# Performance work log

Hardware: AMD Instinct MI355X
Metric: run time of the kernel (lower is better)

Reference implementation:

```python
import jax, jax.numpy as jnp
import numpy as np

C = 128
K = 5
M = 150000   # num vertices
NF = 300000  # num faces
D = 192      # volume side
NEG_SLOPE = 0.2


def _x_shift(K):
    # Exactly replicates the torch module's grid construction.
    grid = np.linspace(-K // 2, K // 2, K)
    grid_3d = np.stack(np.meshgrid(grid, grid, grid), axis=0).transpose(2, 1, 3, 0)
    return jnp.asarray(grid_3d.reshape(-1, 3), jnp.float32)  # [K^3, 3]


def _trilinear_border(vol, g):
    # vol: [D1, D2, D3]; g: [N, 3] normalized coords in (x, y, z) order
    # (x -> D3/W, y -> D2/H, z -> D1/D), align_corners=True, padding_mode='border'.
    D1, D2, D3 = vol.shape
    def pix(c, S):
        return jnp.clip((c + 1.0) * 0.5 * (S - 1), 0.0, S - 1.0)
    ix, iy, iz = pix(g[:, 0], D3), pix(g[:, 1], D2), pix(g[:, 2], D1)
    x0f, y0f, z0f = jnp.floor(ix), jnp.floor(iy), jnp.floor(iz)
    wx, wy, wz = ix - x0f, iy - y0f, iz - z0f
    x0 = x0f.astype(jnp.int32); y0 = y0f.astype(jnp.int32); z0 = z0f.astype(jnp.int32)
    x1 = jnp.minimum(x0 + 1, D3 - 1)
    y1 = jnp.minimum(y0 + 1, D2 - 1)
    z1 = jnp.minimum(z0 + 1, D1 - 1)
    c000 = vol[z0, y0, x0]; c001 = vol[z0, y0, x1]
    c010 = vol[z0, y1, x0]; c011 = vol[z0, y1, x1]
    c100 = vol[z1, y0, x0]; c101 = vol[z1, y0, x1]
    c110 = vol[z1, y1, x0]; c111 = vol[z1, y1, x1]
    c00 = c000 * (1 - wx) + c001 * wx
    c01 = c010 * (1 - wx) + c011 * wx
    c10 = c100 * (1 - wx) + c101 * wx
    c11 = c110 * (1 - wx) + c111 * wx
    c0 = c00 * (1 - wy) + c01 * wy
    c1 = c10 * (1 - wy) + c11 * wy
    return c0 * (1 - wz) + c1 * wz


def _leaky(x):
    return jnp.where(x >= 0, x, NEG_SLOPE * x)


def setup_inputs() -> dict:
    key = jax.random.key(0)
    ks = jax.random.split(key, 9)
    v = jax.random.uniform(ks[0], (1, M, 3), jnp.float32, -0.9, 0.9)
    f = jax.random.randint(ks[1], (1, NF, 3), 0, M, jnp.int32)
    V = jax.random.normal(ks[2], (1, 1, D, D, D), jnp.float32)
    def init(k, shape, fan):
        return jax.random.normal(k, shape, jnp.float32) / np.sqrt(fan).astype(np.float32)
    Wconv = init(ks[3], (C, 1, K, K, K), K ** 3)
    bconv = jnp.zeros((C,), jnp.float32)
    Wlfc = init(ks[4], (C, C), C)
    blfc = jnp.zeros((C,), jnp.float32)
    W1 = init(ks[5], (C, 6), 6)
    b1 = jnp.zeros((C,), jnp.float32)
    W2 = init(ks[6], (4 * C, 2 * C), 2 * C)
    b2 = jnp.zeros((4 * C,), jnp.float32)
    W3 = init(ks[7], (2 * C, 4 * C), 4 * C)
    b3 = jnp.zeros((2 * C,), jnp.float32)
    return dict(v=v, f=f, V=V, Wconv=Wconv, bconv=bconv, Wlfc=Wlfc, blfc=blfc,
                W1=W1, b1=b1, W2=W2, b2=b2, W3=W3, b3=b3)


def reference(v, f, V, Wconv, bconv, Wlfc, blfc, W1, b1, W2, b2, W3, b3):
    m = v.shape[1]
    D1, D2, D3 = V.shape[2], V.shape[3], V.shape[4]
    Dm = max(D1, D2, D3)
    rescale = jnp.array([D3 / Dm, D2 / Dm, D1 / Dm], jnp.float32)
    x_shift = _x_shift(K)  # [K^3, 3]

    # --- cube sampling (Q = n_scale = 1), done under no_grad in torch ---
    pts = (v[0][:, None, :] + x_shift / Dm * 2.0) / rescale  # [m, K^3, 3]
    cubes = _trilinear_border(V[0, 0], pts.reshape(-1, 3)).reshape(m, K ** 3)
    cubes = jax.lax.stop_gradient(cubes)

    # --- localconv: Conv3d with full-size kernel == GEMM over flattened cube ---
    z_local = cubes @ Wconv.reshape(C, -1).T + bconv      # [m, C]
    z_local = _leaky(z_local)
    z_local = _leaky(z_local @ Wlfc.T + blfc)             # [m, C]

    # --- vertex normals (area-weighted face-normal accumulation, pytorch3d style) ---
    faces = f[0]
    vv = v[0]
    p0, p1, p2 = vv[faces[:, 0]], vv[faces[:, 1]], vv[faces[:, 2]]
    fn = jnp.cross(p1 - p0, p2 - p0)
    vn = jnp.zeros_like(vv)
    vn = vn.at[faces[:, 0]].add(fn).at[faces[:, 1]].add(fn).at[faces[:, 2]].add(fn)
    vn = vn / jnp.maximum(jnp.linalg.norm(vn, axis=-1, keepdims=True), 1e-6)

    # --- point-wise MLP fusion ---
    x = jnp.concatenate([v, vn[None]], axis=2)            # [1, m, 6]
    z_point = _leaky(x @ W1.T + b1)                       # [1, m, C]
    z = jnp.concatenate([z_point, z_local[None]], axis=2) # [1, m, 2C]
    z = _leaky(z @ W2.T + b2)                             # [1, m, 4C]
    z = _leaky(z @ W3.T + b3)                             # [1, m, 2C]
    return z
```

## Files before the change

kernel.cpp:

```cpp
#include <hip/hip_runtime.h>
#include <hip/hip_fp16.h>

#define NEG_SLOPE 0.2f

using f16x8 = __attribute__((ext_vector_type(8))) _Float16;
using f32x4 = __attribute__((ext_vector_type(4))) float;

__device__ __forceinline__ float leakyf(float x) { return x >= 0.f ? x : NEG_SLOPE * x; }

__device__ __forceinline__ void gload_lds16(const void* g, void* l) {
    __builtin_amdgcn_global_load_lds(
        (const __attribute__((address_space(1))) unsigned int*)g,
        (__attribute__((address_space(3))) unsigned int*)l, 16, 0, 0);
}

#define MFMA16(a, b, c) __builtin_amdgcn_mfma_f32_16x16x32_f16(a, b, c, 0, 0, 0)

__global__ __launch_bounds__(256)
void fn_kernel(const float* __restrict__ v, const int* __restrict__ f,
               float4* __restrict__ fn4, int nf) {
    int i = blockIdx.x * 256 + threadIdx.x;
    if (i >= nf) return;
    int i0 = f[3 * i], i1 = f[3 * i + 1], i2 = f[3 * i + 2];
    float p0x = v[3 * i0], p0y = v[3 * i0 + 1], p0z = v[3 * i0 + 2];
    float ux = v[3 * i1] - p0x, uy = v[3 * i1 + 1] - p0y, uz = v[3 * i1 + 2] - p0z;
    float wx = v[3 * i2] - p0x, wy = v[3 * i2 + 1] - p0y, wz = v[3 * i2 + 2] - p0z;
    fn4[i] = make_float4(uy * wz - uz * wy, uz * wx - ux * wz, ux * wy - uy * wx, 0.f);
}

__global__ __launch_bounds__(256)
void inc_hist_kernel(const int* __restrict__ f, unsigned* __restrict__ gh, int NE) {
    __shared__ unsigned h[1024];
    const int t = threadIdx.x, blk = blockIdx.x;
    h[t] = 0; h[t + 256] = 0; h[t + 512] = 0; h[t + 768] = 0;
    __syncthreads();
    int base = blk * 4096;
#pragma unroll
    for (int k = 0; k < 16; ++k) {
        int idx = base + k * 256 + t;
        if (idx < NE) atomicAdd(&h[((unsigned)f[idx]) >> 8], 1u);
    }
    __syncthreads();
#pragma unroll
    for (int k = 0; k < 4; ++k) { int b = t + k * 256; gh[(size_t)blk * 1024 + b] = h[b]; }
}

__global__ __launch_bounds__(256)
void row_scan_kernel(unsigned* __restrict__ gh, unsigned* __restrict__ binTotals, int NB) {
    __shared__ unsigned s[256];
    __shared__ unsigned carrySh;
    const int bin = blockIdx.x, t = threadIdx.x;
    if (t == 0) carrySh = 0;
    __syncthreads();
    for (int base = 0; base < NB; base += 256) {
        unsigned c = carrySh;
        int i = base + t;
        unsigned val = (i < NB) ? gh[(size_t)i * 1024 + bin] : 0;
        s[t] = val;
        __syncthreads();
        for (int d = 1; d < 256; d <<= 1) {
            unsigned x = (t >= d) ? s[t - d] : 0;
            __syncthreads();
            s[t] += x;
            __syncthreads();
        }
        if (i < NB) gh[(size_t)i * 1024 + bin] = s[t] - val + c;
        if (t == 255) carrySh = c + s[255];
        __syncthreads();
    }
    if (t == 0) binTotals[bin] = carrySh;
}

__global__ __launch_bounds__(1024)
void bin_scan_kernel(const unsigned* __restrict__ binTotals, unsigned* __restrict__ binstart) {
    __shared__ unsigned s[1024];
    int t = threadIdx.x;
    unsigned val = binTotals[t];
    s[t] = val;
    __syncthreads();
    for (int d = 1; d < 1024; d <<= 1) {
        unsigned x = (t >= d) ? s[t - d] : 0;
        __syncthreads();
        s[t] += x;
        __syncthreads();
    }
    binstart[t] = s[t] - val;
    if (t == 1023) binstart[1024] = s[1023];
}

__global__ __launch_bounds__(256)
void inc_scatter_kernel(const int* __restrict__ f, const unsigned* __restrict__ gh,
                        const unsigned* __restrict__ binstart,
                        unsigned* __restrict__ sortedV, unsigned* __restrict__ sortedE,
                        int NE) {
    __shared__ unsigned loc[1024];
    const int t = threadIdx.x, blk = blockIdx.x;
#pragma unroll
    for (int k = 0; k < 4; ++k) {
        int b = t + k * 256;
        loc[b] = gh[(size_t)blk * 1024 + b] + binstart[b];
    }
    __syncthreads();
    int base = blk * 4096;
#pragma unroll
    for (int k = 0; k < 16; ++k) {
        int idx = base + k * 256 + t;
        if (idx < NE) {
            unsigned vv = (unsigned)f[idx];
            unsigned pos = atomicAdd(&loc[vv >> 8], 1u);
            sortedV[pos] = vv;
            sortedE[pos] = (unsigned)idx;
        }
    }
}

__global__ __launch_bounds__(256)
void vn_gather_kernel(const unsigned* __restrict__ sortedV, const unsigned* __restrict__ sortedE,
                      const float4* __restrict__ fn4, const unsigned* __restrict__ binstart,
                      float* __restrict__ vn, int M) {
    __shared__ float acc[768];
    const int t = threadIdx.x, b = blockIdx.x;
    acc[t] = 0.f; acc[t + 256] = 0.f; acc[t + 512] = 0.f;
    __syncthreads();
    unsigned s = binstart[b], e = binstart[b + 1];
    for (unsigned i = s + t; i < e; i += 256) {
        unsigned vv = sortedV[i];
        float4 fn = fn4[sortedE[i] / 3];
        int lv = (int)(vv & 255u) * 3;
        atomicAdd(&acc[lv + 0], fn.x);
        atomicAdd(&acc[lv + 1], fn.y);
        atomicAdd(&acc[lv + 2], fn.z);
    }
    __syncthreads();
    int gv = b * 256 + t;
    if (gv < M) {
        vn[3 * gv + 0] = acc[t * 3 + 0];
        vn[3 * gv + 1] = acc[t * 3 + 1];
        vn[3 * gv + 2] = acc[t * 3 + 2];
    }
}

__global__ __launch_bounds__(256)
void code_hist_kernel(const float* __restrict__ v, int* __restrict__ codes,
                      int* __restrict__ hist, int M) {
    int i = blockIdx.x * 256 + threadIdx.x;
    if (i >= M) return;
    int cx = min(max((int)((v[3 * i + 0] + 1.f) * 8.f), 0), 15);
    int cy = min(max((int)((v[3 * i + 1] + 1.f) * 8.f), 0), 15);
    int cz = min(max((int)((v[3 * i + 2] + 1.f) * 8.f), 0), 15);
    int code = 0;
#pragma unroll
    for (int b = 0; b < 4; ++b)
        code |= (((cx >> b) & 1) << (3 * b)) | (((cy >> b) & 1) << (3 * b + 1)) |
                (((cz >> b) & 1) << (3 * b + 2));
    codes[i] = code;
    atomicAdd(&hist[code], 1);
}

__global__ __launch_bounds__(1024)
void scan_kernel(const int* __restrict__ hist, int* __restrict__ offs) {
    __shared__ int s[1024];
    int t = threadIdx.x;
    int v0 = hist[4 * t], v1 = hist[4 * t + 1], v2 = hist[4 * t + 2], v3 = hist[4 * t + 3];
    int sum = v0 + v1 + v2 + v3;
    s[t] = sum;
    __syncthreads();
    for (int d = 1; d < 1024; d <<= 1) {
        int val = (t >= d) ? s[t - d] : 0;
        __syncthreads();
        s[t] += val;
        __syncthreads();
    }
    int excl = s[t] - sum;
    offs[4 * t + 0] = excl;
    offs[4 * t + 1] = excl + v0;
    offs[4 * t + 2] = excl + v0 + v1;
    offs[4 * t + 3] = excl + v0 + v1 + v2;
}

__global__ __launch_bounds__(256)
void scatter_kernel(const int* __restrict__ codes, int* __restrict__ offs,
                    int* __restrict__ perm, int M) {
    int i = blockIdx.x * 256 + threadIdx.x;
    if (i >= M) return;
    int pos = atomicAdd(&offs[codes[i]], 1);
    perm[pos] = i;
}

__global__ __launch_bounds__(256)
void sample_kernel(const float* __restrict__ v, const float* __restrict__ vol,
                   const int* __restrict__ perm,
                   __half* __restrict__ cubes, int m_start, int cnt, int nwg) {
    __shared__ float bbox[2][392];
    __shared__ int pi0[2][16];
    __shared__ float pw[2][16];
    const int half = threadIdx.x >> 7;
    const int q = threadIdx.x & 127;
    int q8 = nwg >> 3, r8 = nwg & 7;
    int xcd = blockIdx.x & 7, idxb = blockIdx.x >> 3;
    int bid = (xcd < r8 ? xcd * (q8 + 1) : r8 * (q8 + 1) + (xcd - r8) * q8) + idxb;
    int ml = bid * 2 + half;
    bool valid = ml < cnt;
    int m = valid ? perm[m_start + ml] : 0;

    if (valid && q < 15) {
        int axis = q / 5, idx = q - 5 * axis;
        float g = -3.f + 1.25f * (float)idx;
        float p = v[3 * m + axis] + g / 192.f * 2.f;
        float pos = fminf(fmaxf((p + 1.f) * 0.5f * 191.f, 0.f), 191.f);
        float fl = floorf(pos);
        pi0[half][q] = (int)fl;
        pw[half][q] = pos - fl;
    }
    __syncthreads();
    if (valid) {
        int xlo = pi0[half][0], ylo = pi0[half][5], zlo = pi0[half][10];
        for (int i = q; i < 392; i += 128) {
            int dx = i & 7;
            int dy = (i >> 3) % 7;
            int dz = i / 56;
            int X = min(xlo + dx, 191), Y = min(ylo + dy, 191), Z = min(zlo + dz, 191);
            bbox[half][i] = vol[Z * 36864 + Y * 192 + X];
        }
    }
    __syncthreads();
    if (!valid) return;
    __half* dst = cubes + (size_t)ml * 128;
    if (q >= 125) { dst[q] = __float2half(0.f); return; }
    int a = q % 5, b = (q / 5) % 5, c = q / 25;
    int xlo = pi0[half][0], ylo = pi0[half][5], zlo = pi0[half][10];
    int gx0 = pi0[half][a], gy0 = pi0[half][5 + b], gz0 = pi0[half][10 + c];
    float wxv = pw[half][a], wyv = pw[half][5 + b], wzv = pw[half][10 + c];
    int x0 = gx0 - xlo, y0 = gy0 - ylo, z0 = gz0 - zlo;
    int x1 = min(gx0 + 1, 191) - xlo;
    int y1 = min(gy0 + 1, 191) - ylo;
    int z1 = min(gz0 + 1, 191) - zlo;
    const float* bb = bbox[half];
    int b00 = (z0 * 7 + y0) * 8, b01 = (z0 * 7 + y1) * 8;
    int b10 = (z1 * 7 + y0) * 8, b11 = (z1 * 7 + y1) * 8;
    float c000 = bb[b00 + x0], c001 = bb[b00 + x1];
    float c010 = bb[b01 + x0], c011 = bb[b01 + x1];
    float c100 = bb[b10 + x0], c101 = bb[b10 + x1];
    float c110 = bb[b11 + x0], c111 = bb[b11 + x1];
    float omx = 1.f - wxv, omy = 1.f - wyv, omz = 1.f - wzv;
    float c00 = c000 * omx + c001 * wxv;
    float c01 = c010 * omx + c011 * wxv;
    float c10 = c100 * omx + c101 * wxv;
    float c11 = c110 * omx + c111 * wxv;
    float c0 = c00 * omy + c01 * wyv;
    float c1 = c10 * omy + c11 * wyv;
    dst[25 * a + 5 * b + c] = __float2half(c0 * omz + c1 * wzv);
}

__global__ __launch_bounds__(256)
void prep_weights(const float* __restrict__ Wconv, const float* __restrict__ Wlfc,
                  const float* __restrict__ W2, const float* __restrict__ W3,
                  __half* __restrict__ wpadh, __half* __restrict__ wlfch,
                  __half* __restrict__ w2h, __half* __restrict__ w3h) {
    int b = blockIdx.x, t = threadIdx.x;
    if (b < 64) {
        int i = b * 256 + t; int ch = i >> 7, k = i & 127;
        wpadh[i] = __float2half(k < 125 ? Wconv[ch * 125 + k] : 0.f);
    } else if (b < 128) {
        int i = (b - 64) * 256 + t; wlfch[i] = __float2half(Wlfc[i]);
    } else if (b < 640) {
        int i = (b - 128) * 256 + t; w2h[i] = __float2half(W2[i]);
    } else {
        int i = (b - 640) * 256 + t; w3h[i] = __float2half(W3[i]);
    }
}

__global__ __launch_bounds__(256)
void point_kernel(const float* __restrict__ v, const float* __restrict__ vn,
                  const int* __restrict__ perm,
                  const float* __restrict__ W1, const float* __restrict__ b1,
                  __half* __restrict__ zcat, int m_start, int cnt) {
    int ml = blockIdx.x * 2 + (threadIdx.x >> 7);
    if (ml >= cnt) return;
    int n = threadIdx.x & 127;
    int m = perm[m_start + ml];
    float x0 = v[3 * m], x1 = v[3 * m + 1], x2 = v[3 * m + 2];
    float nx = vn[3 * m], ny = vn[3 * m + 1], nz = vn[3 * m + 2];
    float nrm = fmaxf(sqrtf(nx * nx + ny * ny + nz * nz), 1e-6f);
    nx /= nrm; ny /= nrm; nz /= nrm;
    const float* w = W1 + n * 6;
    float z = b1[n] + x0 * w[0] + x1 * w[1] + x2 * w[2] + nx * w[3] + ny * w[4] + nz * w[5];
    zcat[(size_t)ml * 256 + n] = __float2half(leakyf(z));
}

__global__ __launch_bounds__(256)
void convlfc_kernel(const __half* __restrict__ cubes, const __half* __restrict__ wconvh,
                    const float* __restrict__ bconv, const __half* __restrict__ wlfch,
                    const float* __restrict__ blfc, __half* __restrict__ zcat) {
    __shared__ __half Zt[128 * 128];
    __shared__ __half As[128 * 64];
    __shared__ __half Bs[128 * 64];
    const int t = threadIdx.x;
    const int lane = t & 63, wave = t >> 6;
    const int lr = lane & 15, lg = lane >> 4;
    const int wm = wave >> 1, wn = wave & 1;
    const int m0 = blockIdx.x * 128;
    const int srow = t >> 3;
    const int scb = ((t & 7) << 4) ^ (((t >> 3) & 7) << 4);
    const int swz = (lr & 7) << 4;

    const __half* Ag = cubes + (size_t)(m0 + srow) * 128 + (scb >> 1);
    const __half* Bg = wconvh + (size_t)srow * 128 + (scb >> 1);
    __half* Al = As + wave * 512;
    __half* Bl = Bs + wave * 512;
    const char* aB = (const char*)As + (wm * 64 + lr) * 128;
    const char* bB = (const char*)Bs + (wn * 64 + lr) * 128;

    f32x4 acc[4][4] = {};
    for (int kc = 0; kc < 128; kc += 64) {
#pragma unroll
        for (int i = 0; i < 4; ++i) {
            gload_lds16(Ag + (size_t)i * 32 * 128 + kc, Al + i * 2048);
            gload_lds16(Bg + (size_t)i * 32 * 128 + kc, Bl + i * 2048);
        }
        __syncthreads();
#pragma unroll
        for (int kk = 0; kk < 2; ++kk) {
            const int ko = (kk * 64 + lg * 16) ^ swz;
            f16x8 af[4], bf[4];
#pragma unroll
            for (int fx = 0; fx < 4; ++fx) {
                af[fx] = *(const f16x8*)(aB + fx * 2048 + ko);
                bf[fx] = *(const f16x8*)(bB + fx * 2048 + ko);
            }
#pragma unroll
            for (int fm = 0; fm < 4; ++fm)
#pragma unroll
                for (int fn = 0; fn < 4; ++fn)
                    acc[fm][fn] = MFMA16(af[fm], bf[fn], acc[fm][fn]);
        }
        __syncthreads();
    }
#pragma unroll
    for (int fm = 0; fm < 4; ++fm) {
#pragma unroll
        for (int fn = 0; fn < 4; ++fn) {
            int col = wn * 64 + fn * 16 + lr;
            float bias = bconv[col];
#pragma unroll
            for (int r = 0; r < 4; ++r) {
                int row = wm * 64 + fm * 16 + lg * 4 + r;
                float val = leakyf(acc[fm][fn][r] + bias);
                *(__half*)((char*)Zt + row * 256 + ((2 * col) ^ ((row & 7) << 4))) = __float2half(val);
            }
        }
    }
    __syncthreads();

    const __half* Bg2 = wlfch + (size_t)srow * 128 + (scb >> 1);
    const char* zR = (const char*)Zt + (wm * 64 + lr) * 256;
    f32x4 acc2[4][4] = {};
    for (int kc = 0; kc < 128; kc += 64) {
#pragma unroll
        for (int i = 0; i < 4; ++i)
            gload_lds16(Bg2 + (size_t)i * 32 * 128 + kc, Bl + i * 2048);
        __syncthreads();
#pragma unroll
        for (int kk = 0; kk < 2; ++kk) {
            const int kb = kc * 2 + kk * 64 + lg * 16;
            const int ko = (kk * 64 + lg * 16) ^ swz;
            f16x8 af[4], bf[4];
#pragma unroll
            for (int fx = 0; fx < 4; ++fx) {
                af[fx] = *(const f16x8*)(zR + fx * 4096 + (kb ^ swz));
                bf[fx] = *(const f16x8*)(bB + fx * 2048 + ko);
            }
#pragma unroll
            for (int fm = 0; fm < 4; ++fm)
#pragma unroll
                for (int fn = 0; fn < 4; ++fn)
                    acc2[fm][fn] = MFMA16(af[fm], bf[fn], acc2[fm][fn]);
        }
        __syncthreads();
    }
#pragma unroll
    for (int fm = 0; fm < 4; ++fm) {
#pragma unroll
        for (int fn = 0; fn < 4; ++fn) {
            int col = wn * 64 + fn * 16 + lr;
            float bias = blfc[col];
#pragma unroll
            for (int r = 0; r < 4; ++r) {
                int row = m0 + wm * 64 + fm * 16 + lg * 4 + r;
                zcat[(size_t)row * 256 + 128 + col] = __float2half(leakyf(acc2[fm][fn][r] + bias));
            }
        }
    }
}

template<bool F32OUT>
__global__ __launch_bounds__(256)
void gemm_wide(const __half* __restrict__ A, const __half* __restrict__ W,
               const float* __restrict__ bias, void* __restrict__ outp,
               int K, int Meff, int OS, int OC, const int* __restrict__ rowmap) {
    __shared__ __half As[4096];
    __shared__ __half Bs[16384];
    const int t = threadIdx.x;
    const int lane = t & 63, wave = t >> 6;
    const int lr = lane & 15, lg = lane >> 4;
    const int m0 = blockIdx.x * 64, n0 = blockIdx.y * 256;

    const int srow = t >> 3;
    const int scb = ((t & 7) << 4) ^ (((t >> 3) & 7) << 4);
    const __half* Ag = A + (size_t)(m0 + srow) * K + (scb >> 1);
    const __half* Wg = W + (size_t)(n0 + srow) * K + (scb >> 1);
    __half* Al = As + wave * 512;
    __half* Bl = Bs + wave * 512;

    const int swz = (lr & 7) << 4;
    const char* aB = (const char*)As + lr * 128;
    const char* bB = (const char*)Bs + (wave * 64 + lr) * 128;
    const int k0 = (lg * 16) ^ swz;
    const int k1 = (64 + lg * 16) ^ swz;

    f32x4 acc[4][4] = {};

    for (int kc = 0; kc < K; kc += 64) {
#pragma unroll
        for (int i = 0; i < 2; ++i)
            gload_lds16(Ag + (size_t)i * 32 * K + kc, Al + i * 2048);
#pragma unroll
        for (int i = 0; i < 8; ++i)
            gload_lds16(Wg + (size_t)i * 32 * K + kc, Bl + i * 2048);
        __syncthreads();
        f16x8 af[4], bf[4];
#pragma unroll
        for (int fx = 0; fx < 4; ++fx) {
            af[fx] = *(const f16x8*)(aB + fx * 2048 + k0);
            bf[fx] = *(const f16x8*)(bB + fx * 2048 + k0);
        }
#pragma unroll
        for (int fm = 0; fm < 4; ++fm)
#pragma unroll
            for (int fn = 0; fn < 4; ++fn)
                acc[fm][fn] = MFMA16(af[fm], bf[fn], acc[fm][fn]);
#pragma unroll
        for (int fx = 0; fx < 4; ++fx) {
            af[fx] = *(const f16x8*)(aB + fx * 2048 + k1);
            bf[fx] = *(const f16x8*)(bB + fx * 2048 + k1);
        }
#pragma unroll
        for (int fm = 0; fm < 4; ++fm)
#pragma unroll
            for (int fn = 0; fn < 4; ++fn)
                acc[fm][fn] = MFMA16(af[fm], bf[fn], acc[fm][fn]);
        __syncthreads();
    }

    float bv[4];
#pragma unroll
    for (int fn = 0; fn < 4; ++fn) bv[fn] = bias[n0 + wave * 64 + fn * 16 + lr];
    const int rbase = m0 + lg * 4;
    const int cbase = OC + n0 + wave * 64 + lr;
#pragma unroll
    for (int fm = 0; fm < 4; ++fm) {
#pragma unroll
        for (int r = 0; r < 4; ++r) {
            int row = rbase + fm * 16 + r;
            if (row < Meff) {
                size_t orow = (size_t)(rowmap ? rowmap[row] : row);
#pragma unroll
                for (int fn = 0; fn < 4; ++fn) {
                    float val = leakyf(acc[fm][fn][r] + bv[fn]);
                    if (F32OUT)
                        ((float*)outp)[orow * OS + cbase + fn * 16] = val;
                    else
                        ((__half*)outp)[orow * OS + cbase + fn * 16] = __float2half(val);
                }
            }
        }
    }
}

extern "C" void kernel_launch(void* const* d_in, const int* in_sizes, int n_in,
                              void* d_out, int out_size, void* d_ws, size_t ws_size,
                              hipStream_t stream) {
    const float* v = (const float*)d_in[0];
    const int* f = (const int*)d_in[1];
    const float* vol = (const float*)d_in[2];
    const float* Wconv = (const float*)d_in[3];
    const float* bconv = (const float*)d_in[4];
    const float* Wlfc = (const float*)d_in[5];
    const float* blfc = (const float*)d_in[6];
    const float* W1 = (const float*)d_in[7];
    const float* b1 = (const float*)d_in[8];
    const float* W2 = (const float*)d_in[9];
    const float* b2 = (const float*)d_in[10];
    const float* W3 = (const float*)d_in[11];
    const float* b3 = (const float*)d_in[12];
    float* out = (float*)d_out;
    const int M = in_sizes[0] / 3;
    const int NF = in_sizes[1] / 3;
    const int NE = 3 * NF;
    const int NB = (NE + 4095) / 4096;

    char* base = (char*)d_ws;
    float* vn = (float*)base;
    size_t off = ((size_t)M * 12 + 255) & ~(size_t)255;
    int* codes = (int*)(base + off); off += ((size_t)M * 4 + 255) & ~(size_t)255;
    int* perm  = (int*)(base + off); off += ((size_t)M * 4 + 255) & ~(size_t)255;
    int* hist  = (int*)(base + off); off += 4096 * 4;
    int* offs  = (int*)(base + off); off += 4096 * 4;
    float4* fn4 = (float4*)(base + off); off += (size_t)NF * 16;
    unsigned* sortedV = (unsigned*)(base + off); off += ((size_t)NE * 4 + 255) & ~(size_t)255;
    unsigned* sortedE = (unsigned*)(base + off); off += ((size_t)NE * 4 + 255) & ~(size_t)255;
    unsigned* gh = (unsigned*)(base + off); off += ((size_t)1024 * NB * 4 + 255) & ~(size_t)255;
    unsigned* binstart = (unsigned*)(base + off); off += 1032 * 4;
    unsigned* binTotals = (unsigned*)(base + off); off += 1024 * 4;
    __half* wpadh = (__half*)(base + off); off += 32768;
    __half* wlfch = (__half*)(base + off); off += 32768;
    __half* w2h = (__half*)(base + off); off += 262144;
    __half* w3h = (__half*)(base + off); off += 262144;
    size_t avail = ws_size > off ? ws_size - off : 0;
    size_t Mpad = ((size_t)M + 127) & ~(size_t)127;
    size_t chm = (avail / 1792) & ~(size_t)127;
    if (chm > Mpad) chm = Mpad;
    if (chm < 128) chm = 128;
    __half* cubes = (__half*)(base + off);
    __half* zcat = cubes + chm * 128;
    __half* h = zcat + chm * 256;

    fn_kernel<<<(NF + 255) / 256, 256, 0, stream>>>(v, f, fn4, NF);
    inc_hist_kernel<<<NB, 256, 0, stream>>>(f, gh, NE);
    row_scan_kernel<<<1024, 256, 0, stream>>>(gh, binTotals, NB);
    bin_scan_kernel<<<1, 1024, 0, stream>>>(binTotals, binstart);
    inc_scatter_kernel<<<NB, 256, 0, stream>>>(f, gh, binstart, sortedV, sortedE, NE);
    vn_gather_kernel<<<(M + 255) / 256, 256, 0, stream>>>(sortedV, sortedE, fn4, binstart, vn, M);

    hipMemsetAsync(hist, 0, 4096 * 4, stream);
    code_hist_kernel<<<(M + 255) / 256, 256, 0, stream>>>(v, codes, hist, M);
    scan_kernel<<<1, 1024, 0, stream>>>(hist, offs);
    scatter_kernel<<<(M + 255) / 256, 256, 0, stream>>>(codes, offs, perm, M);
    prep_weights<<<1152, 256, 0, stream>>>(Wconv, Wlfc, W2, W3, wpadh, wlfch, w2h, w3h);

    for (size_t ms = 0; ms < (size_t)M; ms += chm) {
        size_t rem = (size_t)M - ms;
        int cnt = (int)(rem < chm ? rem : chm);
        int mb = (cnt + 127) / 128;
        int mb64 = (cnt + 63) / 64;
        int nblk = (cnt + 1) / 2;
        sample_kernel<<<nblk, 256, 0, stream>>>(v, vol, perm, cubes, (int)ms, cnt, nblk);
        convlfc_kernel<<<mb, 256, 0, stream>>>(cubes, wpadh, bconv, wlfch, blfc, zcat);
        point_kernel<<<(cnt + 1) / 2, 256, 0, stream>>>(v, vn, perm, W1, b1, zcat, (int)ms, cnt);
        gemm_wide<false><<<dim3(mb64, 2), 256, 0, stream>>>(zcat, w2h, b2, h, 256, mb64 * 64, 512, 0, nullptr);
        gemm_wide<true><<<dim3(mb64, 1), 256, 0, stream>>>(h, w3h, b3, out, 512, cnt, 256, 0, perm + ms);
    }
}
```

Baseline: 504.3 us.

## Double-buffer LDS tiles in gemm_wide and repack sample bbox gather

```diff
diff --git a/kernel.cpp b/kernel.cpp
--- a/kernel.cpp
+++ b/kernel.cpp
@@ -191,7 +191,7 @@
 void sample_kernel(const float* __restrict__ v, const float* __restrict__ vol,
                    const int* __restrict__ perm,
                    __half* __restrict__ cubes, int m_start, int cnt, int nwg) {
-    __shared__ float bbox[2][392];
+    __shared__ float bbox[2][448];
     __shared__ int pi0[2][16];
     __shared__ float pw[2][16];
     const int half = threadIdx.x >> 7;
@@ -215,12 +215,21 @@
     __syncthreads();
     if (valid) {
         int xlo = pi0[half][0], ylo = pi0[half][5], zlo = pi0[half][10];
-        for (int i = q; i < 392; i += 128) {
-            int dx = i & 7;
-            int dy = (i >> 3) % 7;
-            int dz = i / 56;
-            int X = min(xlo + dx, 191), Y = min(ylo + dy, 191), Z = min(zlo + dz, 191);
-            bbox[half][i] = vol[Z * 36864 + Y * 192 + X];
+        int j = q & 63;
+        int dy = j >> 3, dx = j & 7;
+        if (dy < 7) {
+            int X = min(xlo + dx, 191);
+            int Y = min(ylo + dy, 191);
+            int rowoff = dy * 9 + dx;
+            const float* volYX = vol + Y * 192 + X;
+#pragma unroll
+            for (int k = 0; k < 4; ++k) {
+                int pz = (q >> 6) + k * 2;
+                if (pz < 7) {
+                    int Z = min(zlo + pz, 191);
+                    bbox[half][pz * 63 + rowoff] = volYX[Z * 36864];
+                }
+            }
         }
     }
     __syncthreads();
@@ -236,8 +245,8 @@
     int y1 = min(gy0 + 1, 191) - ylo;
     int z1 = min(gz0 + 1, 191) - zlo;
     const float* bb = bbox[half];
-    int b00 = (z0 * 7 + y0) * 8, b01 = (z0 * 7 + y1) * 8;
-    int b10 = (z1 * 7 + y0) * 8, b11 = (z1 * 7 + y1) * 8;
+    int b00 = z0 * 63 + y0 * 9, b01 = z0 * 63 + y1 * 9;
+    int b10 = z1 * 63 + y0 * 9, b11 = z1 * 63 + y1 * 9;
     float c000 = bb[b00 + x0], c001 = bb[b00 + x1];
     float c010 = bb[b01 + x0], c011 = bb[b01 + x1];
     float c100 = bb[b10 + x0], c101 = bb[b10 + x1];
@@ -398,8 +407,8 @@
 void gemm_wide(const __half* __restrict__ A, const __half* __restrict__ W,
                const float* __restrict__ bias, void* __restrict__ outp,
                int K, int Meff, int OS, int OC, const int* __restrict__ rowmap) {
-    __shared__ __half As[4096];
-    __shared__ __half Bs[16384];
+    __shared__ __half As[2][4096];
+    __shared__ __half Bs[2][16384];
     const int t = threadIdx.x;
     const int lane = t & 63, wave = t >> 6;
     const int lr = lane & 15, lg = lane >> 4;
@@ -409,25 +418,41 @@
     const int scb = ((t & 7) << 4) ^ (((t >> 3) & 7) << 4);
     const __half* Ag = A + (size_t)(m0 + srow) * K + (scb >> 1);
     const __half* Wg = W + (size_t)(n0 + srow) * K + (scb >> 1);
-    __half* Al = As + wave * 512;
-    __half* Bl = Bs + wave * 512;
 
     const int swz = (lr & 7) << 4;
-    const char* aB = (const char*)As + lr * 128;
-    const char* bB = (const char*)Bs + (wave * 64 + lr) * 128;
+    const int aOff = lr * 128;
+    const int bOff = (wave * 64 + lr) * 128;
     const int k0 = (lg * 16) ^ swz;
     const int k1 = (64 + lg * 16) ^ swz;
 
     f32x4 acc[4][4] = {};
 
+    {
+        __half* Al = As[0] + wave * 512;
+        __half* Bl = Bs[0] + wave * 512;
+#pragma unroll
+        for (int i = 0; i < 2; ++i)
+            gload_lds16(Ag + (size_t)i * 32 * K, Al + i * 2048);
+#pragma unroll
+        for (int i = 0; i < 8; ++i)
+            gload_lds16(Wg + (size_t)i * 32 * K, Bl + i * 2048);
+    }
+    __syncthreads();
+
+    int cur = 0;
     for (int kc = 0; kc < K; kc += 64) {
-#pragma unroll
-        for (int i = 0; i < 2; ++i)
-            gload_lds16(Ag + (size_t)i * 32 * K + kc, Al + i * 2048);
-#pragma unroll
-        for (int i = 0; i < 8; ++i)
-            gload_lds16(Wg + (size_t)i * 32 * K + kc, Bl + i * 2048);
-        __syncthreads();
+        if (kc + 64 < K) {
+            __half* Al = As[cur ^ 1] + wave * 512;
+            __half* Bl = Bs[cur ^ 1] + wave * 512;
+#pragma unroll
+            for (int i = 0; i < 2; ++i)
+                gload_lds16(Ag + (size_t)i * 32 * K + kc + 64, Al + i * 2048);
+#pragma unroll
+            for (int i = 0; i < 8; ++i)
+                gload_lds16(Wg + (size_t)i * 32 * K + kc + 64, Bl + i * 2048);
+        }
+        const char* aB = (const char*)As[cur] + aOff;
+        const char* bB = (const char*)Bs[cur] + bOff;
         f16x8 af[4], bf[4];
 #pragma unroll
         for (int fx = 0; fx < 4; ++fx) {
@@ -450,6 +475,7 @@
             for (int fn = 0; fn < 4; ++fn)
                 acc[fm][fn] = MFMA16(af[fm], bf[fn], acc[fm][fn]);
         __syncthreads();
+        cur ^= 1;
     }
 
     float bv[4];
```

Measured after the change: 504.8 us. About the same (+0.1%).

## Merge independent prelude kernels into combined launches and restructure sample bbox loads

Applied to the files above, without the earlier changes.

```diff
diff --git a/kernel.cpp b/kernel.cpp
--- a/kernel.cpp
+++ b/kernel.cpp
@@ -17,75 +17,146 @@
 #define MFMA16(a, b, c) __builtin_amdgcn_mfma_f32_16x16x32_f16(a, b, c, 0, 0, 0)
 
 __global__ __launch_bounds__(256)
-void fn_kernel(const float* __restrict__ v, const int* __restrict__ f,
-               float4* __restrict__ fn4, int nf) {
-    int i = blockIdx.x * 256 + threadIdx.x;
-    if (i >= nf) return;
-    int i0 = f[3 * i], i1 = f[3 * i + 1], i2 = f[3 * i + 2];
-    float p0x = v[3 * i0], p0y = v[3 * i0 + 1], p0z = v[3 * i0 + 2];
-    float ux = v[3 * i1] - p0x, uy = v[3 * i1 + 1] - p0y, uz = v[3 * i1 + 2] - p0z;
-    float wx = v[3 * i2] - p0x, wy = v[3 * i2 + 1] - p0y, wz = v[3 * i2 + 2] - p0z;
-    fn4[i] = make_float4(uy * wz - uz * wy, uz * wx - ux * wz, ux * wy - uy * wx, 0.f);
-}
-
-__global__ __launch_bounds__(256)
-void inc_hist_kernel(const int* __restrict__ f, unsigned* __restrict__ gh, int NE) {
+void prelude1_kernel(const float* __restrict__ v, const int* __restrict__ f,
+                     float4* __restrict__ fn4, int NF, int NE,
+                     unsigned* __restrict__ gh, int fnB, int ihB, int chB,
+                     int* __restrict__ codes, int* __restrict__ hist, int M,
+                     const float* __restrict__ Wconv, const float* __restrict__ Wlfc,
+                     const float* __restrict__ W2, const float* __restrict__ W3,
+                     __half* __restrict__ wpadh, __half* __restrict__ wlfch,
+                     __half* __restrict__ w2h, __half* __restrict__ w3h) {
     __shared__ unsigned h[1024];
-    const int t = threadIdx.x, blk = blockIdx.x;
-    h[t] = 0; h[t + 256] = 0; h[t + 512] = 0; h[t + 768] = 0;
-    __syncthreads();
-    int base = blk * 4096;
-#pragma unroll
-    for (int k = 0; k < 16; ++k) {
-        int idx = base + k * 256 + t;
-        if (idx < NE) atomicAdd(&h[((unsigned)f[idx]) >> 8], 1u);
-    }
-    __syncthreads();
-#pragma unroll
-    for (int k = 0; k < 4; ++k) { int b = t + k * 256; gh[(size_t)blk * 1024 + b] = h[b]; }
-}
-
-__global__ __launch_bounds__(256)
-void row_scan_kernel(unsigned* __restrict__ gh, unsigned* __restrict__ binTotals, int NB) {
+    const int t = threadIdx.x;
+    int b = blockIdx.x;
+    if (b < fnB) {
+        int i = b * 256 + t;
+        if (i >= NF) return;
+        int i0 = f[3 * i], i1 = f[3 * i + 1], i2 = f[3 * i + 2];
+        float p0x = v[3 * i0], p0y = v[3 * i0 + 1], p0z = v[3 * i0 + 2];
+        float ux = v[3 * i1] - p0x, uy = v[3 * i1 + 1] - p0y, uz = v[3 * i1 + 2] - p0z;
+        float wx = v[3 * i2] - p0x, wy = v[3 * i2 + 1] - p0y, wz = v[3 * i2 + 2] - p0z;
+        fn4[i] = make_float4(uy * wz - uz * wy, uz * wx - ux * wz, ux * wy - uy * wx, 0.f);
+    } else if (b < fnB + ihB) {
+        int blk = b - fnB;
+        h[t] = 0; h[t + 256] = 0; h[t + 512] = 0; h[t + 768] = 0;
+        __syncthreads();
+        int base = blk * 4096;
+#pragma unroll
+        for (int k = 0; k < 16; ++k) {
+            int idx = base + k * 256 + t;
+            if (idx < NE) atomicAdd(&h[((unsigned)f[idx]) >> 8], 1u);
+        }
+        __syncthreads();
+#pragma unroll
+        for (int k = 0; k < 4; ++k) { int bb = t + k * 256; gh[(size_t)blk * 1024 + bb] = h[bb]; }
+    } else if (b < fnB + ihB + chB) {
+        int i = (b - fnB - ihB) * 256 + t;
+        if (i >= M) return;
+        int cx = min(max((int)((v[3 * i + 0] + 1.f) * 8.f), 0), 15);
+        int cy = min(max((int)((v[3 * i + 1] + 1.f) * 8.f), 0), 15);
+        int cz = min(max((int)((v[3 * i + 2] + 1.f) * 8.f), 0), 15);
+        int code = 0;
+#pragma unroll
+        for (int bb = 0; bb < 4; ++bb)
+            code |= (((cx >> bb) & 1) << (3 * bb)) | (((cy >> bb) & 1) << (3 * bb + 1)) |
+                    (((cz >> bb) & 1) << (3 * bb + 2));
+        codes[i] = code;
+        atomicAdd(&hist[code], 1);
+    } else {
+        int bw = b - fnB - ihB - chB;
+        if (bw < 64) {
+            int i = bw * 256 + t; int ch = i >> 7, k = i & 127;
+            wpadh[i] = __float2half(k < 125 ? Wconv[ch * 125 + k] : 0.f);
+        } else if (bw < 128) {
+            int i = (bw - 64) * 256 + t; wlfch[i] = __float2half(Wlfc[i]);
+        } else if (bw < 640) {
+            int i = (bw - 128) * 256 + t; w2h[i] = __float2half(W2[i]);
+        } else {
+            int i = (bw - 640) * 256 + t; w3h[i] = __float2half(W3[i]);
+        }
+    }
+}
+
+__global__ __launch_bounds__(256)
+void prelude2_kernel(unsigned* __restrict__ gh, unsigned* __restrict__ binTotals, int NB,
+                     const int* __restrict__ hist, int* __restrict__ offs) {
     __shared__ unsigned s[256];
     __shared__ unsigned carrySh;
-    const int bin = blockIdx.x, t = threadIdx.x;
-    if (t == 0) carrySh = 0;
-    __syncthreads();
-    for (int base = 0; base < NB; base += 256) {
-        unsigned c = carrySh;
-        int i = base + t;
-        unsigned val = (i < NB) ? gh[(size_t)i * 1024 + bin] : 0;
-        s[t] = val;
-        __syncthreads();
-        for (int d = 1; d < 256; d <<= 1) {
-            unsigned x = (t >= d) ? s[t - d] : 0;
+    const int t = threadIdx.x;
+    if (blockIdx.x < 1024) {
+        const int bin = blockIdx.x;
+        if (t == 0) carrySh = 0;
+        __syncthreads();
+        for (int base = 0; base < NB; base += 256) {
+            unsigned c = carrySh;
+            int i = base + t;
+            unsigned val = (i < NB) ? gh[(size_t)i * 1024 + bin] : 0;
+            s[t] = val;
             __syncthreads();
-            s[t] += x;
+            for (int d = 1; d < 256; d <<= 1) {
+                unsigned x = (t >= d) ? s[t - d] : 0;
+                __syncthreads();
+                s[t] += x;
+                __syncthreads();
+            }
+            if (i < NB) gh[(size_t)i * 1024 + bin] = s[t] - val + c;
+            if (t == 255) carrySh = c + s[255];
             __syncthreads();
         }
-        if (i < NB) gh[(size_t)i * 1024 + bin] = s[t] - val + c;
-        if (t == 255) carrySh = c + s[255];
-        __syncthreads();
-    }
-    if (t == 0) binTotals[bin] = carrySh;
-}
-
-__global__ __launch_bounds__(1024)
-void bin_scan_kernel(const unsigned* __restrict__ binTotals, unsigned* __restrict__ binstart) {
-    __shared__ unsigned s[1024];
-    int t = threadIdx.x;
-    unsigned val = binTotals[t];
-    s[t] = val;
-    __syncthreads();
-    for (int d = 1; d < 1024; d <<= 1) {
-        unsigned x = (t >= d) ? s[t - d] : 0;
-        __syncthreads();
-        s[t] += x;
-        __syncthreads();
-    }
-    binstart[t] = s[t] - val;
-    if (t == 1023) binstart[1024] = s[1023];
+        if (t == 0) binTotals[bin] = carrySh;
+    } else {
+        if (t == 0) carrySh = 0;
+        __syncthreads();
+        for (int base = 0; base < 4096; base += 256) {
+            unsigned c = carrySh;
+            unsigned val = (unsigned)hist[base + t];
+            s[t] = val;
+            __syncthreads();
+            for (int d = 1; d < 256; d <<= 1) {
+                unsigned x = (t >= d) ? s[t - d] : 0;
+                __syncthreads();
+                s[t] += x;
+                __syncthreads();
+            }
+            offs[base + t] = (int)(s[t] - val + c);
+            if (t == 255) carrySh = c + s[255];
+            __syncthreads();
+        }
+    }
+}
+
+__global__ __launch_bounds__(256)
+void prelude3_kernel(const unsigned* __restrict__ binTotals, unsigned* __restrict__ binstart,
+                     const int* __restrict__ codes, int* __restrict__ offs,
+                     int* __restrict__ perm, int M) {
+    __shared__ unsigned s[256];
+    __shared__ unsigned carrySh;
+    const int t = threadIdx.x;
+    if (blockIdx.x == 0) {
+        if (t == 0) carrySh = 0;
+        __syncthreads();
+        for (int base = 0; base < 1024; base += 256) {
+            unsigned c = carrySh;
+            unsigned val = binTotals[base + t];
+            s[t] = val;
+            __syncthreads();
+            for (int d = 1; d < 256; d <<= 1) {
+                unsigned x = (t >= d) ? s[t - d] : 0;
+                __syncthreads();
+                s[t] += x;
+                __syncthreads();
+            }
+            binstart[base + t] = s[t] - val + c;
+            if (t == 255) carrySh = c + s[255];
+            __syncthreads();
+        }
+        if (t == 0) binstart[1024] = carrySh;
+    } else {
+        int i = (blockIdx.x - 1) * 256 + t;
+        if (i >= M) return;
+        int pos = atomicAdd(&offs[codes[i]], 1);
+        perm[pos] = i;
+    }
 }
 
 __global__ __launch_bounds__(256)
@@ -141,57 +212,10 @@
 }
 
 __global__ __launch_bounds__(256)
-void code_hist_kernel(const float* __restrict__ v, int* __restrict__ codes,
-                      int* __restrict__ hist, int M) {
-    int i = blockIdx.x * 256 + threadIdx.x;
-    if (i >= M) return;
-    int cx = min(max((int)((v[3 * i + 0] + 1.f) * 8.f), 0), 15);
-    int cy = min(max((int)((v[3 * i + 1] + 1.f) * 8.f), 0), 15);
-    int cz = min(max((int)((v[3 * i + 2] + 1.f) * 8.f), 0), 15);
-    int code = 0;
-#pragma unroll
-    for (int b = 0; b < 4; ++b)
-        code |= (((cx >> b) & 1) << (3 * b)) | (((cy >> b) & 1) << (3 * b + 1)) |
-                (((cz >> b) & 1) << (3 * b + 2));
-    codes[i] = code;
-    atomicAdd(&hist[code], 1);
-}
-
-__global__ __launch_bounds__(1024)
-void scan_kernel(const int* __restrict__ hist, int* __restrict__ offs) {
-    __shared__ int s[1024];
-    int t = threadIdx.x;
-    int v0 = hist[4 * t], v1 = hist[4 * t + 1], v2 = hist[4 * t + 2], v3 = hist[4 * t + 3];
-    int sum = v0 + v1 + v2 + v3;
-    s[t] = sum;
-    __syncthreads();
-    for (int d = 1; d < 1024; d <<= 1) {
-        int val = (t >= d) ? s[t - d] : 0;
-        __syncthreads();
-        s[t] += val;
-        __syncthreads();
-    }
-    int excl = s[t] - sum;
-    offs[4 * t + 0] = excl;
-    offs[4 * t + 1] = excl + v0;
-    offs[4 * t + 2] = excl + v0 + v1;
-    offs[4 * t + 3] = excl + v0 + v1 + v2;
-}
-
-__global__ __launch_bounds__(256)
-void scatter_kernel(const int* __restrict__ codes, int* __restrict__ offs,
-                    int* __restrict__ perm, int M) {
-    int i = blockIdx.x * 256 + threadIdx.x;
-    if (i >= M) return;
-    int pos = atomicAdd(&offs[codes[i]], 1);
-    perm[pos] = i;
-}
-
-__global__ __launch_bounds__(256)
 void sample_kernel(const float* __restrict__ v, const float* __restrict__ vol,
                    const int* __restrict__ perm,
                    __half* __restrict__ cubes, int m_start, int cnt, int nwg) {
-    __shared__ float bbox[2][392];
+    __shared__ float bbox[2][448];
     __shared__ int pi0[2][16];
     __shared__ float pw[2][16];
     const int half = threadIdx.x >> 7;
@@ -215,12 +239,21 @@
     __syncthreads();
     if (valid) {
         int xlo = pi0[half][0], ylo = pi0[half][5], zlo = pi0[half][10];
-        for (int i = q; i < 392; i += 128) {
-            int dx = i & 7;
-            int dy = (i >> 3) % 7;
-            int dz = i / 56;
-            int X = min(xlo + dx, 191), Y = min(ylo + dy, 191), Z = min(zlo + dz, 191);
-            bbox[half][i] = vol[Z * 36864 + Y * 192 + X];
+        int j = q & 63;
+        int dy = j >> 3, dx = j & 7;
+        if (dy < 7) {
+            int X = min(xlo + dx, 191);
+            int Y = min(ylo + dy, 191);
+            int rowoff = dy * 9 + dx;
+            const float* volYX = vol + Y * 192 + X;
+#pragma unroll
+            for (int k = 0; k < 4; ++k) {
+                int pz = (q >> 6) + k * 2;
+                if (pz < 7) {
+                    int Z = min(zlo + pz, 191);
+                    bbox[half][pz * 63 + rowoff] = volYX[Z * 36864];
+                }
+            }
         }
     }
     __syncthreads();
@@ -236,8 +269,8 @@
     int y1 = min(gy0 + 1, 191) - ylo;
     int z1 = min(gz0 + 1, 191) - zlo;
     const float* bb = bbox[half];
-    int b00 = (z0 * 7 + y0) * 8, b01 = (z0 * 7 + y1) * 8;
-    int b10 = (z1 * 7 + y0) * 8, b11 = (z1 * 7 + y1) * 8;
+    int b00 = z0 * 63 + y0 * 9, b01 = z0 * 63 + y1 * 9;
+    int b10 = z1 * 63 + y0 * 9, b11 = z1 * 63 + y1 * 9;
     float c000 = bb[b00 + x0], c001 = bb[b00 + x1];
     float c010 = bb[b01 + x0], c011 = bb[b01 + x1];
     float c100 = bb[b10 + x0], c101 = bb[b10 + x1];
@@ -253,49 +286,31 @@
 }
 
 __global__ __launch_bounds__(256)
-void prep_weights(const float* __restrict__ Wconv, const float* __restrict__ Wlfc,
-                  const float* __restrict__ W2, const float* __restrict__ W3,
-                  __half* __restrict__ wpadh, __half* __restrict__ wlfch,
-                  __half* __restrict__ w2h, __half* __restrict__ w3h) {
-    int b = blockIdx.x, t = threadIdx.x;
-    if (b < 64) {
-        int i = b * 256 + t; int ch = i >> 7, k = i & 127;
-        wpadh[i] = __float2half(k < 125 ? Wconv[ch * 125 + k] : 0.f);
-    } else if (b < 128) {
-        int i = (b - 64) * 256 + t; wlfch[i] = __float2half(Wlfc[i]);
-    } else if (b < 640) {
-        int i = (b - 128) * 256 + t; w2h[i] = __float2half(W2[i]);
-    } else {
-        int i = (b - 640) * 256 + t; w3h[i] = __float2half(W3[i]);
-    }
-}
-
-__global__ __launch_bounds__(256)
-void point_kernel(const float* __restrict__ v, const float* __restrict__ vn,
-                  const int* __restrict__ perm,
-                  const float* __restrict__ W1, const float* __restrict__ b1,
-                  __half* __restrict__ zcat, int m_start, int cnt) {
-    int ml = blockIdx.x * 2 + (threadIdx.x >> 7);
-    if (ml >= cnt) return;
-    int n = threadIdx.x & 127;
-    int m = perm[m_start + ml];
-    float x0 = v[3 * m], x1 = v[3 * m + 1], x2 = v[3 * m + 2];
-    float nx = vn[3 * m], ny = vn[3 * m + 1], nz = vn[3 * m + 2];
-    float nrm = fmaxf(sqrtf(nx * nx + ny * ny + nz * nz), 1e-6f);
-    nx /= nrm; ny /= nrm; nz /= nrm;
-    const float* w = W1 + n * 6;
-    float z = b1[n] + x0 * w[0] + x1 * w[1] + x2 * w[2] + nx * w[3] + ny * w[4] + nz * w[5];
-    zcat[(size_t)ml * 256 + n] = __float2half(leakyf(z));
-}
-
-__global__ __launch_bounds__(256)
-void convlfc_kernel(const __half* __restrict__ cubes, const __half* __restrict__ wconvh,
-                    const float* __restrict__ bconv, const __half* __restrict__ wlfch,
-                    const float* __restrict__ blfc, __half* __restrict__ zcat) {
+void convpoint_kernel(const __half* __restrict__ cubes, const __half* __restrict__ wconvh,
+                      const float* __restrict__ bconv, const __half* __restrict__ wlfch,
+                      const float* __restrict__ blfc, __half* __restrict__ zcat,
+                      const float* __restrict__ v, const float* __restrict__ vn,
+                      const int* __restrict__ perm,
+                      const float* __restrict__ W1, const float* __restrict__ b1,
+                      int m_start, int cnt, int mb) {
     __shared__ __half Zt[128 * 128];
     __shared__ __half As[128 * 64];
     __shared__ __half Bs[128 * 64];
     const int t = threadIdx.x;
+    if (blockIdx.x >= mb) {
+        int ml = (blockIdx.x - mb) * 2 + (t >> 7);
+        if (ml >= cnt) return;
+        int n = t & 127;
+        int m = perm[m_start + ml];
+        float x0 = v[3 * m], x1 = v[3 * m + 1], x2 = v[3 * m + 2];
+        float nx = vn[3 * m], ny = vn[3 * m + 1], nz = vn[3 * m + 2];
+        float nrm = fmaxf(sqrtf(nx * nx + ny * ny + nz * nz), 1e-6f);
+        nx /= nrm; ny /= nrm; nz /= nrm;
+        const float* w = W1 + n * 6;
+        float z = b1[n] + x0 * w[0] + x1 * w[1] + x2 * w[2] + nx * w[3] + ny * w[4] + nz * w[5];
+        zcat[(size_t)ml * 256 + n] = __float2half(leakyf(z));
+        return;
+    }
     const int lane = t & 63, wave = t >> 6;
     const int lr = lane & 15, lg = lane >> 4;
     const int wm = wave >> 1, wn = wave & 1;
@@ -525,18 +540,17 @@
     __half* zcat = cubes + chm * 128;
     __half* h = zcat + chm * 256;
 
-    fn_kernel<<<(NF + 255) / 256, 256, 0, stream>>>(v, f, fn4, NF);
-    inc_hist_kernel<<<NB, 256, 0, stream>>>(f, gh, NE);
-    row_scan_kernel<<<1024, 256, 0, stream>>>(gh, binTotals, NB);
-    bin_scan_kernel<<<1, 1024, 0, stream>>>(binTotals, binstart);
+    const int fnB = (NF + 255) / 256;
+    const int chB = (M + 255) / 256;
+
+    hipMemsetAsync(hist, 0, 4096 * 4, stream);
+    prelude1_kernel<<<fnB + NB + chB + 1152, 256, 0, stream>>>(
+        v, f, fn4, NF, NE, gh, fnB, NB, chB, codes, hist, M,
+        Wconv, Wlfc, W2, W3, wpadh, wlfch, w2h, w3h);
+    prelude2_kernel<<<1025, 256, 0, stream>>>(gh, binTotals, NB, hist, offs);
+    prelude3_kernel<<<1 + chB, 256, 0, stream>>>(binTotals, binstart, codes, offs, perm, M);
     inc_scatter_kernel<<<NB, 256, 0, stream>>>(f, gh, binstart, sortedV, sortedE, NE);
     vn_gather_kernel<<<(M + 255) / 256, 256, 0, stream>>>(sortedV, sortedE, fn4, binstart, vn, M);
-
-    hipMemsetAsync(hist, 0, 4096 * 4, stream);
-    code_hist_kernel<<<(M + 255) / 256, 256, 0, stream>>>(v, codes, hist, M);
-    scan_kernel<<<1, 1024, 0, stream>>>(hist, offs);
-    scatter_kernel<<<(M + 255) / 256, 256, 0, stream>>>(codes, offs, perm, M);
-    prep_weights<<<1152, 256, 0, stream>>>(Wconv, Wlfc, W2, W3, wpadh, wlfch, w2h, w3h);
 
     for (size_t ms = 0; ms < (size_t)M; ms += chm) {
         size_t rem = (size_t)M - ms;
@@ -545,9 +559,11 @@
         int mb64 = (cnt + 63) / 64;
         int nblk = (cnt + 1) / 2;
         sample_kernel<<<nblk, 256, 0, stream>>>(v, vol, perm, cubes, (int)ms, cnt, nblk);
-        convlfc_kernel<<<mb, 256, 0, stream>>>(cubes, wpadh, bconv, wlfch, blfc, zcat);
-        point_kernel<<<(cnt + 1) / 2, 256, 0, stream>>>(v, vn, perm, W1, b1, zcat, (int)ms, cnt);
-        gemm_wide<false><<<dim3(mb64, 2), 256, 0, stream>>>(zcat, w2h, b2, h, 256, mb64 * 64, 512, 0, nullptr);
-        gemm_wide<true><<<dim3(mb64, 1), 256, 0, stream>>>(h, w3h, b3, out, 512, cnt, 256, 0, perm + ms);
-    }
-}
+        convpoint_kernel<<<mb + (cnt + 1) / 2, 256, 0, stream>>>(
+            cubes, wpadh, bconv, wlfch, blfc, zcat, v, vn, perm, W1, b1, (int)ms, cnt, mb);
+        gemm_wide<false><<<dim3(mb64, 2), 256, 0, stream>>>(
+            zcat, w2h, b2, h, 256, mb64 * 64, 512, 0, nullptr);
+        gemm_wide<true><<<dim3(mb64, 1), 256, 0, stream>>>(
+            h, w3h, b3, out, 512, cnt, 256, 0, perm + ms);
+    }
+}
```

Result: slower. 581.2 us (+15.3%).
